# Optimization experiments

Hardware: AMD Instinct MI355X
Metric: run time of the kernel (lower is better)

The kernel has to match this reference:

```python
import jax, jax.numpy as jnp
import numpy as np

N, E = 50000, 800000
IN_DIM, HID = 11, 128
EPS = 1e-5

def setup_inputs() -> dict:
    key = jax.random.key(0)
    ks = jax.random.split(key, 20)
    def w(k, i, o):
        return jax.random.normal(k, (i, o), jnp.float32) * (1.0 / np.sqrt(i))
    inp = {}
    inp['x'] = jax.random.normal(ks[0], (N, IN_DIM), jnp.float32)
    inp['edge_index'] = jax.random.randint(ks[1], (2, E), 0, N, jnp.int64)
    dims = [(IN_DIM, HID), (HID, HID), (HID, HID)]
    for i, (di, do) in enumerate(dims):
        inp[f'w_l{i}'] = w(ks[2 + 3 * i], di, do)
        inp[f'b_l{i}'] = jnp.zeros((do,), jnp.float32)
        inp[f'w_r{i}'] = w(ks[3 + 3 * i], di, do)
        inp[f'ln_w{i}'] = jnp.ones((do,), jnp.float32)
        inp[f'ln_b{i}'] = jnp.zeros((do,), jnp.float32)
    inp['c_w0'] = w(ks[12], HID, HID // 2)
    inp['c_b0'] = jnp.zeros((HID // 2,), jnp.float32)
    inp['c_w1'] = w(ks[13], HID // 2, 1)
    inp['c_b1'] = jnp.zeros((1,), jnp.float32)
    return inp

def _sage_conv(x, src, dst, w_l, b_l, w_r):
    # PyG SAGEConv (mean aggr): lin_l(mean_{j in N(i)} x_j) + lin_r(x_i)
    n = x.shape[0]
    agg = jax.ops.segment_sum(x[src], dst, num_segments=n)
    cnt = jax.ops.segment_sum(jnp.ones((src.shape[0], 1), x.dtype), dst, num_segments=n)
    agg = agg / jnp.maximum(cnt, 1.0)
    return agg @ w_l + b_l + x @ w_r

def _layernorm(h, w, b):
    mu = jnp.mean(h, axis=-1, keepdims=True)
    var = jnp.mean(jnp.square(h - mu), axis=-1, keepdims=True)
    return (h - mu) * jax.lax.rsqrt(var + EPS) * w + b

def reference(x, edge_index, w_l0, b_l0, w_r0, ln_w0, ln_b0,
              w_l1, b_l1, w_r1, ln_w1, ln_b1,
              w_l2, b_l2, w_r2, ln_w2, ln_b2,
              c_w0, c_b0, c_w1, c_b1):
    src, dst = edge_index[0], edge_index[1]
    layers = [(w_l0, b_l0, w_r0, ln_w0, ln_b0),
              (w_l1, b_l1, w_r1, ln_w1, ln_b1),
              (w_l2, b_l2, w_r2, ln_w2, ln_b2)]
    for i, (wl, bl, wr, gw, gb) in enumerate(layers):
        h = _sage_conv(x, src, dst, wl, bl, wr)
        h = jax.nn.relu(_layernorm(h, gw, gb))
        # dropout is identity in eval mode
        if i > 0 and h.shape == x.shape:
            h = h + x
        x = h
    h = jax.nn.relu(x @ c_w0 + c_b0)
    out = h @ c_w1 + c_b1
    return out.squeeze(-1)
```

## Files before the change

kernel.cpp:

```cpp
#include <hip/hip_runtime.h>
#include <hip/hip_fp16.h>

#define HID 128

typedef _Float16 h2_t __attribute__((ext_vector_type(2)));
typedef _Float16 half8 __attribute__((ext_vector_type(8)));
typedef float f32x4 __attribute__((ext_vector_type(4)));

static __device__ __forceinline__ float fdot2(__half2 a, __half2 b, float c) {
    return __builtin_amdgcn_fdot2(__builtin_bit_cast(h2_t, a), __builtin_bit_cast(h2_t, b), c, false);
}

__global__ __launch_bounds__(256) void zero_kernel(int4* __restrict__ p, int n4) {
    int i = blockIdx.x * 256 + threadIdx.x;
    if (i < n4) p[i] = make_int4(0, 0, 0, 0);
}

__global__ __launch_bounds__(256) void deg_kernel(const int* __restrict__ ei,
                                                  int* __restrict__ deg, int E, int n) {
    int grp  = blockIdx.x & 7;
    int blk  = blockIdx.x >> 3;
    int nblk = gridDim.x >> 3;
    int lo = (int)(((long long)n * grp) >> 3);
    int hi = (int)(((long long)n * (grp + 1)) >> 3);
    for (int e = blk * 256 + threadIdx.x; e < E; e += nblk * 256) {
        int dst = ei[E + e];
        if (dst >= lo && dst < hi) atomicAdd(&deg[dst], 1);
    }
}

__global__ __launch_bounds__(256) void part_kernel(const int* __restrict__ deg,
                                                   int* __restrict__ part, int n) {
    int i = blockIdx.x * 256 + threadIdx.x;
    int v = (i < n) ? deg[i] : 0;
    #pragma unroll
    for (int m = 1; m < 64; m <<= 1) v += __shfl_xor(v, m);
    __shared__ int w[4];
    int lane = threadIdx.x & 63, wv = threadIdx.x >> 6;
    if (lane == 0) w[wv] = v;
    __syncthreads();
    if (threadIdx.x == 0) part[blockIdx.x] = w[0] + w[1] + w[2] + w[3];
}

__global__ __launch_bounds__(1024) void scanpart_kernel(int* __restrict__ part, int nb) {
    __shared__ int s[1024];
    int t = threadIdx.x;
    int v = (t < nb) ? part[t] : 0;
    int orig = v;
    s[t] = v;
    __syncthreads();
    for (int off = 1; off < 1024; off <<= 1) {
        int u = (t >= off) ? s[t - off] : 0;
        __syncthreads();
        s[t] += u;
        __syncthreads();
    }
    if (t < nb) part[t] = s[t] - orig;
}

__global__ __launch_bounds__(256) void rp_kernel(const int* __restrict__ deg,
                                                 const int* __restrict__ part,
                                                 int* __restrict__ rp,
                                                 int* __restrict__ cursor, int n) {
    int tid = threadIdx.x, lane = tid & 63, wv = tid >> 6;
    int i = blockIdx.x * 256 + tid;
    int v = (i < n) ? deg[i] : 0;
    int orig = v;
    #pragma unroll
    for (int off = 1; off < 64; off <<= 1) {
        int t = __shfl_up(v, off);
        if (lane >= off) v += t;
    }
    __shared__ int wsum[4];
    if (lane == 63) wsum[wv] = v;
    __syncthreads();
    int wbase = 0;
    #pragma unroll
    for (int w = 0; w < 4; ++w) if (w < wv) wbase += wsum[w];
    int excl = part[blockIdx.x] + wbase + v - orig;
    if (i < n) { rp[i] = excl; cursor[i] = excl; }
    if (i == n - 1) rp[n] = excl + orig;
}

__global__ __launch_bounds__(256) void fill_kernel(const int* __restrict__ ei,
                                                   int* __restrict__ cursor,
                                                   int* __restrict__ csr_src, int E, int n) {
    int grp  = blockIdx.x & 7;
    int blk  = blockIdx.x >> 3;
    int nblk = gridDim.x >> 3;
    int lo = (int)(((long long)n * grp) >> 3);
    int hi = (int)(((long long)n * (grp + 1)) >> 3);
    for (int e = blk * 256 + threadIdx.x; e < E; e += nblk * 256) {
        int dst = ei[E + e];
        if (dst >= lo && dst < hi) {
            int pos = atomicAdd(&cursor[dst], 1);
            csr_src[pos] = ei[e];
        }
    }
}

__global__ __launch_bounds__(256) void aggp_kernel(const int* __restrict__ rp,
                                                   const int* __restrict__ ci,
                                                   const __half* __restrict__ h16,
                                                   __half* __restrict__ agg16, int n) {
    int node = (blockIdx.x * 256 + threadIdx.x) >> 6;
    if (node >= n) return;
    int lane = threadIdx.x & 63;
    int half = lane >> 5;
    int c4 = (lane & 31) * 4;
    int beg = rp[node], end = rp[node + 1];
    float4 A0 = make_float4(0.f, 0.f, 0.f, 0.f);
    float4 A1 = make_float4(0.f, 0.f, 0.f, 0.f);
    float4 A2 = make_float4(0.f, 0.f, 0.f, 0.f);
    float4 A3 = make_float4(0.f, 0.f, 0.f, 0.f);
    int j = beg + half;
    for (; j + 6 < end; j += 8) {
        int s0 = ci[j], s1 = ci[j + 2], s2 = ci[j + 4], s3 = ci[j + 6];
        float2 r0 = *(const float2*)(h16 + (size_t)s0 * HID + c4);
        float2 r1 = *(const float2*)(h16 + (size_t)s1 * HID + c4);
        float2 r2 = *(const float2*)(h16 + (size_t)s2 * HID + c4);
        float2 r3 = *(const float2*)(h16 + (size_t)s3 * HID + c4);
        const __half2* p0 = (const __half2*)&r0;
        const __half2* p1 = (const __half2*)&r1;
        const __half2* p2 = (const __half2*)&r2;
        const __half2* p3 = (const __half2*)&r3;
        float2 l0 = __half22float2(p0[0]), h0 = __half22float2(p0[1]);
        float2 l1 = __half22float2(p1[0]), h1 = __half22float2(p1[1]);
        float2 l2 = __half22float2(p2[0]), h2 = __half22float2(p2[1]);
        float2 l3 = __half22float2(p3[0]), h3 = __half22float2(p3[1]);
        A0.x += l0.x; A0.y += l0.y; A0.z += h0.x; A0.w += h0.y;
        A1.x += l1.x; A1.y += l1.y; A1.z += h1.x; A1.w += h1.y;
        A2.x += l2.x; A2.y += l2.y; A2.z += h2.x; A2.w += h2.y;
        A3.x += l3.x; A3.y += l3.y; A3.z += h3.x; A3.w += h3.y;
    }
    for (; j < end; j += 2) {
        int s0 = ci[j];
        float2 r0 = *(const float2*)(h16 + (size_t)s0 * HID + c4);
        const __half2* p0 = (const __half2*)&r0;
        float2 l0 = __half22float2(p0[0]), h0 = __half22float2(p0[1]);
        A0.x += l0.x; A0.y += l0.y; A0.z += h0.x; A0.w += h0.y;
    }
    float ax = A0.x + A1.x + A2.x + A3.x;
    float ay = A0.y + A1.y + A2.y + A3.y;
    float az = A0.z + A1.z + A2.z + A3.z;
    float aw = A0.w + A1.w + A2.w + A3.w;
    ax += __shfl_xor(ax, 32);
    ay += __shfl_xor(ay, 32);
    az += __shfl_xor(az, 32);
    aw += __shfl_xor(aw, 32);
    if (lane < 32) {
        float inv = 1.0f / fmaxf((float)(end - beg), 1.0f);
        __half2 o01 = __floats2half2_rn(ax * inv, ay * inv);
        __half2 o23 = __floats2half2_rn(az * inv, aw * inv);
        float2 pack;
        ((__half2*)&pack)[0] = o01;
        ((__half2*)&pack)[1] = o23;
        *(float2*)(agg16 + (size_t)node * HID + c4) = pack;
    }
}

__global__ __launch_bounds__(256) void layer0_kernel(
    const float* __restrict__ x, const int* __restrict__ rp, const int* __restrict__ ci,
    const float* __restrict__ w_l, const float* __restrict__ b_l, const float* __restrict__ w_r,
    const float* __restrict__ ln_w, const float* __restrict__ ln_b,
    __half* __restrict__ h16, int n)
{
    int node = (blockIdx.x * 256 + threadIdx.x) >> 6;
    int lane = threadIdx.x & 63;
    if (node >= n) return;
    int beg = rp[node], end = rp[node + 1];
    float a[11];
    #pragma unroll
    for (int k = 0; k < 11; ++k) a[k] = 0.f;
    for (int j = beg + lane; j < end; j += 64) {
        int src = ci[j];
        const float* xr = x + (size_t)src * 11;
        #pragma unroll
        for (int k = 0; k < 11; ++k) a[k] += xr[k];
    }
    #pragma unroll
    for (int k = 0; k < 11; ++k) {
        float v = a[k];
        #pragma unroll
        for (int m = 1; m < 64; m <<= 1) v += __shfl_xor(v, m);
        a[k] = v;
    }
    float inv = 1.0f / fmaxf((float)(end - beg), 1.0f);
    float v0 = b_l[lane], v1 = b_l[lane + 64];
    #pragma unroll
    for (int k = 0; k < 11; ++k) {
        float ak = a[k] * inv;
        float xi = x[(size_t)node * 11 + k];
        v0 += ak * w_l[k * HID + lane]      + xi * w_r[k * HID + lane];
        v1 += ak * w_l[k * HID + lane + 64] + xi * w_r[k * HID + lane + 64];
    }
    float s = v0 + v1, s2 = v0 * v0 + v1 * v1;
    #pragma unroll
    for (int m = 1; m < 64; m <<= 1) { s += __shfl_xor(s, m); s2 += __shfl_xor(s2, m); }
    float mu  = s * (1.0f / HID);
    float var = s2 * (1.0f / HID) - mu * mu;
    float rstd = rsqrtf(var + 1e-5f);
    float o0 = fmaxf((v0 - mu) * rstd * ln_w[lane]      + ln_b[lane],      0.0f);
    float o1 = fmaxf((v1 - mu) * rstd * ln_w[lane + 64] + ln_b[lane + 64], 0.0f);
    h16[(size_t)node * HID + lane]      = __float2half_rn(o0);
    h16[(size_t)node * HID + lane + 64] = __float2half_rn(o1);
}

__global__ __launch_bounds__(256) void wfrag_kernel(const float* __restrict__ wl,
                                                    const float* __restrict__ wr,
                                                    __half* __restrict__ wf) {
    int idx = blockIdx.x * 256 + threadIdx.x;
    if (idx >= 4096) return;
    int kt = idx >> 9;
    int ct = (idx >> 6) & 7;
    int l  = idx & 63;
    int col = ct * 16 + (l & 15);
    int kbase = kt * 32 + (l >> 4) * 8;
    #pragma unroll
    for (int j = 0; j < 8; ++j) {
        int k = kbase + j;
        const float* W = (k < HID) ? wl : wr;
        int kk = k & (HID - 1);
        wf[(size_t)idx * 8 + j] = __float2half_rn(W[kk * HID + col]);
    }
}

__global__ __launch_bounds__(256) void wpack_cls_kernel(const float* __restrict__ w0,
                                                        __half2* __restrict__ w0p) {
    int idx = blockIdx.x * 256 + threadIdx.x;
    if (idx >= 64 * 64) return;
    int p = idx >> 6, c = idx & 63;
    w0p[idx] = __floats2half2_rn(w0[(2 * p) * 64 + c], w0[(2 * p + 1) * 64 + c]);
}

__global__ __launch_bounds__(256) void layer_kernel(
    const __half* __restrict__ agg16, const __half* __restrict__ h16in,
    const __half* __restrict__ wf, const float* __restrict__ b_l,
    const float* __restrict__ ln_w, const float* __restrict__ ln_b,
    __half* __restrict__ h16out, int n)
{
    __shared__ __half lds[64][264];
    int base = blockIdx.x * 64;
    int tid = threadIdx.x;
    #pragma unroll
    for (int i = 0; i < 8; ++i) {
        int idx = tid + i * 256;
        int row = idx >> 5;
        int c4  = (idx & 31) * 4;
        int node = base + row;
        float2 a = make_float2(0.f, 0.f);
        float2 h = make_float2(0.f, 0.f);
        if (node < n) {
            a = *(const float2*)(agg16 + (size_t)node * HID + c4);
            h = *(const float2*)(h16in + (size_t)node * HID + c4);
        }
        *(float2*)&lds[row][c4]       = a;
        *(float2*)&lds[row][HID + c4] = h;
    }
    __syncthreads();

    int w = tid >> 6;
    int l = tid & 63;
    int g = l >> 4, cl = l & 15;

    f32x4 acc[8];
    #pragma unroll
    for (int ct = 0; ct < 8; ++ct) acc[ct] = (f32x4){0.f, 0.f, 0.f, 0.f};

    #pragma unroll
    for (int kt = 0; kt < 8; ++kt) {
        half8 a = *(const half8*)&lds[w * 16 + cl][kt * 32 + g * 8];
        #pragma unroll
        for (int ct = 0; ct < 8; ++ct) {
            half8 b = *(const half8*)(wf + ((size_t)(kt * 8 + ct) * 64 + l) * 8);
            acc[ct] = __builtin_amdgcn_mfma_f32_16x16x32_f16(a, b, acc[ct], 0, 0, 0);
        }
    }

    float bl8[8], gw8[8], gb8[8];
    #pragma unroll
    for (int ct = 0; ct < 8; ++ct) {
        bl8[ct] = b_l[ct * 16 + cl];
        gw8[ct] = ln_w[ct * 16 + cl];
        gb8[ct] = ln_b[ct * 16 + cl];
    }

    #pragma unroll
    for (int r = 0; r < 4; ++r) {
        int row = w * 16 + g * 4 + r;
        float v[8];
        float s = 0.f, s2 = 0.f;
        #pragma unroll
        for (int ct = 0; ct < 8; ++ct) {
            v[ct] = acc[ct][r] + bl8[ct];
            s += v[ct]; s2 += v[ct] * v[ct];
        }
        #pragma unroll
        for (int m = 1; m < 16; m <<= 1) { s += __shfl_xor(s, m); s2 += __shfl_xor(s2, m); }
        float mu  = s * (1.0f / HID);
        float var = s2 * (1.0f / HID) - mu * mu;
        float rstd = rsqrtf(var + 1e-5f);
        int node = base + row;
        if (node < n) {
            #pragma unroll
            for (int ct = 0; ct < 8; ++ct) {
                float o = fmaxf((v[ct] - mu) * rstd * gw8[ct] + gb8[ct], 0.f)
                          + __half2float(lds[row][HID + ct * 16 + cl]);
                h16out[(size_t)node * HID + ct * 16 + cl] = __float2half_rn(o);
            }
        }
    }
}

__global__ __launch_bounds__(256) void cls_kernel(
    const __half* __restrict__ h, const __half2* __restrict__ w0p, const float* __restrict__ b0,
    const float* __restrict__ w1, const float* __restrict__ b1, float* __restrict__ out, int n)
{
    __shared__ __half2 w0s[64 * 64];
    int tid = threadIdx.x;
    #pragma unroll
    for (int i = 0; i < 16; ++i) w0s[tid + i * 256] = w0p[tid + i * 256];
    __syncthreads();
    int lane = tid & 63, wv = tid >> 6;
    float bb0 = b0[lane], ww1 = w1[lane], bb1 = b1[0];
    #pragma unroll 1
    for (int q = 0; q < 8; ++q) {
        int node = blockIdx.x * 32 + wv * 8 + q;
        if (node >= n) break;
        const __half2* hr = (const __half2*)(h + (size_t)node * HID);
        float s0 = 0.f, s1 = 0.f;
        #pragma unroll
        for (int p = 0; p < 64; p += 2) {
            s0 = fdot2(hr[p],     w0s[(p + 0) * 64 + lane], s0);
            s1 = fdot2(hr[p + 1], w0s[(p + 1) * 64 + lane], s1);
        }
        float s = fmaxf(s0 + s1 + bb0, 0.f);
        float t = s * ww1;
        #pragma unroll
        for (int m = 1; m < 64; m <<= 1) t += __shfl_xor(t, m);
        if (lane == 0) out[node] = t + bb1;
    }
}

extern "C" void kernel_launch(void* const* d_in, const int* in_sizes, int n_in,
                              void* d_out, int out_size, void* d_ws, size_t ws_size,
                              hipStream_t stream) {
    const float* x  = (const float*)d_in[0];
    const int*   ei = (const int*)d_in[1];
    const float* w_l0 = (const float*)d_in[2];
    const float* b_l0 = (const float*)d_in[3];
    const float* w_r0 = (const float*)d_in[4];
    const float* lnw0 = (const float*)d_in[5];
    const float* lnb0 = (const float*)d_in[6];
    const float* w_l1 = (const float*)d_in[7];
    const float* b_l1 = (const float*)d_in[8];
    const float* w_r1 = (const float*)d_in[9];
    const float* lnw1 = (const float*)d_in[10];
    const float* lnb1 = (const float*)d_in[11];
    const float* w_l2 = (const float*)d_in[12];
    const float* b_l2 = (const float*)d_in[13];
    const float* w_r2 = (const float*)d_in[14];
    const float* lnw2 = (const float*)d_in[15];
    const float* lnb2 = (const float*)d_in[16];
    const float* c_w0 = (const float*)d_in[17];
    const float* c_b0 = (const float*)d_in[18];
    const float* c_w1 = (const float*)d_in[19];
    const float* c_b1 = (const float*)d_in[20];
    float* out = (float*)d_out;

    int N = in_sizes[0] / 11;
    int E = in_sizes[1] / 2;
    int nb = (N + 255) / 256;

    int*     deg    = (int*)d_ws;
    int*     rp     = deg + N;
    int*     cursor = rp + (N + 1);
    int*     csr    = cursor + N;
    int*     part   = csr + E;
    __half*  h16    = (__half*)(part + ((nb + 63) & ~63));
    __half*  agg16  = h16 + (size_t)N * HID;
    __half*  wf1    = agg16 + (size_t)N * HID;
    __half*  wf2    = wf1 + 4096 * 8;
    __half2* w0p    = (__half2*)(wf2 + 4096 * 8);

    int n4 = (N + 3) / 4;
    zero_kernel<<<(n4 + 255) / 256, 256, 0, stream>>>((int4*)deg, n4);
    deg_kernel<<<8 * 512, 256, 0, stream>>>(ei, deg, E, N);
    part_kernel<<<nb, 256, 0, stream>>>(deg, part, N);
    scanpart_kernel<<<1, 1024, 0, stream>>>(part, nb);
    rp_kernel<<<nb, 256, 0, stream>>>(deg, part, rp, cursor, N);
    fill_kernel<<<8 * 512, 256, 0, stream>>>(ei, cursor, csr, E, N);
    wfrag_kernel<<<16, 256, 0, stream>>>(w_l1, w_r1, wf1);
    wfrag_kernel<<<16, 256, 0, stream>>>(w_l2, w_r2, wf2);
    wpack_cls_kernel<<<16, 256, 0, stream>>>(c_w0, w0p);

    int nodeBlocks = (N + 3) / 4;

    layer0_kernel<<<nodeBlocks, 256, 0, stream>>>(x, rp, csr, w_l0, b_l0, w_r0, lnw0, lnb0, h16, N);

    aggp_kernel<<<nodeBlocks, 256, 0, stream>>>(rp, csr, h16, agg16, N);
    layer_kernel<<<(N + 63) / 64, 256, 0, stream>>>(agg16, h16, wf1, b_l1, lnw1, lnb1, h16, N);

    aggp_kernel<<<nodeBlocks, 256, 0, stream>>>(rp, csr, h16, agg16, N);
    layer_kernel<<<(N + 63) / 64, 256, 0, stream>>>(agg16, h16, wf2, b_l2, lnw2, lnb2, h16, N);

    cls_kernel<<<(N + 31) / 32, 256, 0, stream>>>(h16, w0p, c_b0, c_w1, c_b1, out, N);
}
```

Before: 280.6 us.

## Split layer-0 neighbor aggregation into a separate per-feature kernel

Moves the layer-0 mean aggregation out of the wavefront-per-node kernel into a new kernel that uses one thread per (node, feature), with a two-way unrolled gather over neighbors. The old version had mostly idle lanes, since average degree is about 16 while a wavefront is 64 lanes, and it needed 11 full butterfly reductions per node. The layer-0 kernel now reads the precomputed fp32 aggregate and broadcasts it with shuffles. This costs an extra launch and an N×11 fp32 buffer round-trip through memory.

```diff
diff --git a/kernel.cpp b/kernel.cpp
--- a/kernel.cpp
+++ b/kernel.cpp
@@ -159,8 +159,27 @@
     }
 }
 
+__global__ __launch_bounds__(256) void agg0_kernel(const float* __restrict__ x,
+                                                   const int* __restrict__ rp,
+                                                   const int* __restrict__ ci,
+                                                   float* __restrict__ agg0, int n) {
+    int idx = blockIdx.x * 256 + threadIdx.x;
+    if (idx >= n * 11) return;
+    int node = idx / 11;
+    int k = idx - node * 11;
+    int beg = rp[node], end = rp[node + 1];
+    float a = 0.f, b = 0.f;
+    int j = beg;
+    for (; j + 1 < end; j += 2) {
+        a += x[(size_t)ci[j] * 11 + k];
+        b += x[(size_t)ci[j + 1] * 11 + k];
+    }
+    if (j < end) a += x[(size_t)ci[j] * 11 + k];
+    agg0[idx] = (a + b) / fmaxf((float)(end - beg), 1.0f);
+}
+
 __global__ __launch_bounds__(256) void layer0_kernel(
-    const float* __restrict__ x, const int* __restrict__ rp, const int* __restrict__ ci,
+    const float* __restrict__ x, const float* __restrict__ agg0,
     const float* __restrict__ w_l, const float* __restrict__ b_l, const float* __restrict__ w_r,
     const float* __restrict__ ln_w, const float* __restrict__ ln_b,
     __half* __restrict__ h16, int n)
@@ -168,31 +187,14 @@
     int node = (blockIdx.x * 256 + threadIdx.x) >> 6;
     int lane = threadIdx.x & 63;
     if (node >= n) return;
-    int beg = rp[node], end = rp[node + 1];
-    float a[11];
-    #pragma unroll
-    for (int k = 0; k < 11; ++k) a[k] = 0.f;
-    for (int j = beg + lane; j < end; j += 64) {
-        int src = ci[j];
-        const float* xr = x + (size_t)src * 11;
-        #pragma unroll
-        for (int k = 0; k < 11; ++k) a[k] += xr[k];
-    }
+    float aggk = (lane < 11) ? agg0[(size_t)node * 11 + lane] : 0.f;
+    float v0 = b_l[lane], v1 = b_l[lane + 64];
     #pragma unroll
     for (int k = 0; k < 11; ++k) {
-        float v = a[k];
-        #pragma unroll
-        for (int m = 1; m < 64; m <<= 1) v += __shfl_xor(v, m);
-        a[k] = v;
-    }
-    float inv = 1.0f / fmaxf((float)(end - beg), 1.0f);
-    float v0 = b_l[lane], v1 = b_l[lane + 64];
-    #pragma unroll
-    for (int k = 0; k < 11; ++k) {
-        float ak = a[k] * inv;
+        float a  = __shfl(aggk, k);
         float xi = x[(size_t)node * 11 + k];
-        v0 += ak * w_l[k * HID + lane]      + xi * w_r[k * HID + lane];
-        v1 += ak * w_l[k * HID + lane + 64] + xi * w_r[k * HID + lane + 64];
+        v0 += a * w_l[k * HID + lane]      + xi * w_r[k * HID + lane];
+        v1 += a * w_l[k * HID + lane + 64] + xi * w_r[k * HID + lane + 64];
     }
     float s = v0 + v1, s2 = v0 * v0 + v1 * v1;
     #pragma unroll
@@ -377,7 +379,8 @@
     int*     cursor = rp + (N + 1);
     int*     csr    = cursor + N;
     int*     part   = csr + E;
-    __half*  h16    = (__half*)(part + ((nb + 63) & ~63));
+    float*   agg0   = (float*)(part + ((nb + 63) & ~63));
+    __half*  h16    = (__half*)(agg0 + (size_t)N * 11);
     __half*  agg16  = h16 + (size_t)N * HID;
     __half*  wf1    = agg16 + (size_t)N * HID;
     __half*  wf2    = wf1 + 4096 * 8;
@@ -396,7 +399,8 @@
 
     int nodeBlocks = (N + 3) / 4;
 
-    layer0_kernel<<<nodeBlocks, 256, 0, stream>>>(x, rp, csr, w_l0, b_l0, w_r0, lnw0, lnb0, h16, N);
+    agg0_kernel<<<((N * 11) + 255) / 256, 256, 0, stream>>>(x, rp, csr, agg0, N);
+    layer0_kernel<<<nodeBlocks, 256, 0, stream>>>(x, agg0, w_l0, b_l0, w_r0, lnw0, lnb0, h16, N);
 
     aggp_kernel<<<nodeBlocks, 256, 0, stream>>>(rp, csr, h16, agg16, N);
     layer_kernel<<<(N + 63) / 64, 256, 0, stream>>>(agg16, h16, wf1, b_l1, lnw1, lnb1, h16, N);
```

New measurement: 279.0 us. Within noise of the previous version (-0.6%).
